# Optimization experiments

Measured on AMD Instinct MI355X. Metric: run time of the kernel, lower is better.

## Reference

```python
import jax, jax.numpy as jnp
import numpy as np

NEG_SLOPE = 0.01  # nn.LeakyReLU default


def setup_inputs() -> dict:
    key = jax.random.key(0)
    k1, k2, k3 = jax.random.split(key, 3)
    N, F_IN, F_OUT = 8192, 128, 64
    h = jax.random.normal(k1, (N, F_IN), dtype=jnp.float32)
    W = jax.random.normal(k2, (F_IN, F_OUT), dtype=jnp.float32) * (1.414 / np.sqrt(F_IN))
    a = jax.random.normal(k3, (2 * F_OUT, 1), dtype=jnp.float32) * (1.414 / np.sqrt(2 * F_OUT))
    return {"h": h, "W": W, "a": a}


def reference(h, W, a):
    # Wh: [N, F_out]
    Wh = h @ W
    F_out = W.shape[1]
    a1 = a[:F_out, 0]   # applies to the "source" (row) node i
    a2 = a[F_out:, 0]   # applies to the "target" (col) node j
    # e[i, j] = leakyrelu(a1 . Wh_i + a2 . Wh_j)  -- algebraic decomposition of
    # the concat-based score; avoids the O(N^2 * 2F) concat tensor.
    f1 = Wh @ a1  # [N]
    f2 = Wh @ a2  # [N]
    e = jax.nn.leaky_relu(f1[:, None] + f2[None, :], negative_slope=NEG_SLOPE)  # [N, N]
    attention = jax.nn.softmax(e, axis=1)
    # dropout is identity in eval mode (training=False)
    h_prime = attention @ Wh  # [N, F_out]
    return jax.nn.elu(h_prime)  # concat=True branch
```

## Files before the change

kernel.cpp:

```cpp
#include <hip/hip_runtime.h>
#include <hip/hip_bf16.h>
#include <stdint.h>

typedef float f32x4 __attribute__((ext_vector_type(4)));
typedef short s16x8 __attribute__((ext_vector_type(8)));
typedef unsigned int u32x4 __attribute__((ext_vector_type(4)));

#define L2E 1.44269504088896f

__device__ __forceinline__ unsigned short f2bf_rne(float f) {
    unsigned int u = __float_as_uint(f);
    u += 0x7fffu + ((u >> 16) & 1u);
    return (unsigned short)(u >> 16);
}

__global__ __launch_bounds__(256) void k1_wh(
    const float* __restrict__ hf,
    const float* __restrict__ Wf,
    const float* __restrict__ af,
    unsigned short* __restrict__ whT,
    float* __restrict__ f1L,
    float* __restrict__ f2L)
{
    __shared__ __align__(16) unsigned short tb[64][72];
    const int tid  = threadIdx.x;
    const int lane = tid & 63;
    const int w    = tid >> 6;
    const int col  = lane & 15;
    const int quad = lane >> 4;
    const int i0   = blockIdx.x * 64;

    f32x4 D[4];
    #pragma unroll
    for (int f = 0; f < 4; ++f) D[f] = (f32x4){0.f, 0.f, 0.f, 0.f};

    const int rowA = i0 + w * 16 + col;
    #pragma unroll
    for (int cs = 0; cs < 4; ++cs) {
        f32x4 h0 = *(const f32x4*)&hf[(size_t)rowA * 128 + cs * 32 + quad * 8];
        f32x4 h1 = *(const f32x4*)&hf[(size_t)rowA * 128 + cs * 32 + quad * 8 + 4];
        s16x8 A;
        #pragma unroll
        for (int jj = 0; jj < 4; ++jj) {
            A[jj]     = (short)f2bf_rne(h0[jj]);
            A[4 + jj] = (short)f2bf_rne(h1[jj]);
        }
        #pragma unroll
        for (int f = 0; f < 4; ++f) {
            s16x8 B;
            #pragma unroll
            for (int jj = 0; jj < 8; ++jj)
                B[jj] = (short)f2bf_rne(Wf[(cs * 32 + quad * 8 + jj) * 64 + f * 16 + col]);
            D[f] = __builtin_amdgcn_mfma_f32_16x16x32_bf16(A, B, D[f], 0, 0, 0);
        }
    }

    float a1v[4], a2v[4];
    #pragma unroll
    for (int f = 0; f < 4; ++f) {
        a1v[f] = af[f * 16 + col];
        a2v[f] = af[64 + f * 16 + col];
    }

    #pragma unroll
    for (int r = 0; r < 4; ++r) {
        float s1 = D[0][r]*a1v[0] + D[1][r]*a1v[1] + D[2][r]*a1v[2] + D[3][r]*a1v[3];
        float s2 = D[0][r]*a2v[0] + D[1][r]*a2v[1] + D[2][r]*a2v[2] + D[3][r]*a2v[3];
        #pragma unroll
        for (int d = 1; d < 16; d <<= 1) {
            s1 += __shfl_xor(s1, d, 64);
            s2 += __shfl_xor(s2, d, 64);
        }
        if (col == 0) {
            int i = i0 + w * 16 + quad * 4 + r;
            f1L[i] = s1 * L2E;
            f2L[i] = s2 * L2E;
        }
        #pragma unroll
        for (int f = 0; f < 4; ++f)
            tb[f * 16 + col][w * 16 + quad * 4 + r] = f2bf_rne(D[f][r]);
    }
    __syncthreads();
    for (int idx = tid; idx < 512; idx += 256) {
        int n = idx >> 3, c8 = (idx & 7) << 3;
        *(u32x4*)&whT[(size_t)n * 8192 + i0 + c8] = *(const u32x4*)&tb[n][c8];
    }
}

__global__ __launch_bounds__(256) void k2_attn(
    const unsigned short* __restrict__ whT,
    const float* __restrict__ f1L,
    const float* __restrict__ f2L,
    float* __restrict__ Apart,
    float* __restrict__ rsumP)
{
    __shared__ __align__(16) unsigned short Bt[64][264];
    __shared__ __align__(16) float f2s[256];
    const int tid  = threadIdx.x;
    const int lane = tid & 63;
    const int w    = tid >> 6;
    const int col  = lane & 15;
    const int quad = lane >> 4;
    const int i0   = blockIdx.x * 64;
    const int jb   = blockIdx.y * 1024;

    const float f1 = f1L[i0 + w * 16 + col];

    f32x4 D0 = (f32x4){0.f,0.f,0.f,0.f}, D1 = D0, D2 = D0, D3 = D0, Ds = D0;
    s16x8 ones;
    #pragma unroll
    for (int jj = 0; jj < 8; ++jj) ones[jj] = (short)0x3f80;

    for (int s = 0; s < 4; ++s) {
        __syncthreads();
        if (tid < 64)
            *(f32x4*)&f2s[tid * 4] = *(const f32x4*)&f2L[jb + (s << 8) + tid * 4];
        for (int idx = tid; idx < 2048; idx += 256) {
            int n = idx >> 5, c = (idx & 31) << 3;
            *(u32x4*)&Bt[n][c] =
                *(const u32x4*)&whT[(size_t)n * 8192 + jb + (s << 8) + c];
        }
        __syncthreads();
        #pragma unroll
        for (int j0 = 0; j0 < 256; j0 += 32) {
            const int jq = j0 + quad * 8;
            f32x4 fa = *(const f32x4*)&f2s[jq];
            f32x4 fb = *(const f32x4*)&f2s[jq + 4];
            unsigned int pb[8];
            #pragma unroll
            for (int e = 0; e < 4; ++e) {
                float u = f1 + fa[e];
                u = fmaxf(u, 0.01f * u);
                u = fminf(fmaxf(u, -126.f), 80.f);
                pb[e] = __float_as_uint(__builtin_amdgcn_exp2f(u));
                float v = f1 + fb[e];
                v = fmaxf(v, 0.01f * v);
                v = fminf(fmaxf(v, -126.f), 80.f);
                pb[4 + e] = __float_as_uint(__builtin_amdgcn_exp2f(v));
            }
            union { u32x4 u4; s16x8 s8; } Au;
            Au.u4[0] = __builtin_amdgcn_perm(pb[1], pb[0], 0x07060302u);
            Au.u4[1] = __builtin_amdgcn_perm(pb[3], pb[2], 0x07060302u);
            Au.u4[2] = __builtin_amdgcn_perm(pb[5], pb[4], 0x07060302u);
            Au.u4[3] = __builtin_amdgcn_perm(pb[7], pb[6], 0x07060302u);
            s16x8 B0 = *(const s16x8*)&Bt[col][jq];
            s16x8 B1 = *(const s16x8*)&Bt[16 + col][jq];
            s16x8 B2 = *(const s16x8*)&Bt[32 + col][jq];
            s16x8 B3 = *(const s16x8*)&Bt[48 + col][jq];
            D0 = __builtin_amdgcn_mfma_f32_16x16x32_bf16(Au.s8, B0, D0, 0, 0, 0);
            D1 = __builtin_amdgcn_mfma_f32_16x16x32_bf16(Au.s8, B1, D1, 0, 0, 0);
            D2 = __builtin_amdgcn_mfma_f32_16x16x32_bf16(Au.s8, B2, D2, 0, 0, 0);
            D3 = __builtin_amdgcn_mfma_f32_16x16x32_bf16(Au.s8, B3, D3, 0, 0, 0);
            Ds = __builtin_amdgcn_mfma_f32_16x16x32_bf16(Au.s8, ones, Ds, 0, 0, 0);
        }
    }

    float* Ap = Apart + (size_t)blockIdx.y * 524288;
    #pragma unroll
    for (int r = 0; r < 4; ++r) {
        int i = i0 + w * 16 + quad * 4 + r;
        Ap[(size_t)i * 64 +      col] = D0[r];
        Ap[(size_t)i * 64 + 16 + col] = D1[r];
        Ap[(size_t)i * 64 + 32 + col] = D2[r];
        Ap[(size_t)i * 64 + 48 + col] = D3[r];
        if (col == 0) rsumP[blockIdx.y * 8192 + i] = Ds[r];
    }
}

__global__ __launch_bounds__(256) void k3_combine(
    const float* __restrict__ Apart,
    const float* __restrict__ rsumP,
    float* __restrict__ out)
{
    int gid = blockIdx.x * 256 + threadIdx.x;
    int i  = gid >> 4;
    int c4 = (gid & 15) << 2;
    f32x4 num = (f32x4){0.f, 0.f, 0.f, 0.f};
    float den = 0.f;
    #pragma unroll
    for (int s = 0; s < 8; ++s) {
        num += *(const f32x4*)&Apart[(size_t)s * 524288 + (size_t)i * 64 + c4];
        den += rsumP[s * 8192 + i];
    }
    float rden = 1.f / den;
    f32x4 o;
    #pragma unroll
    for (int e = 0; e < 4; ++e) {
        float v = num[e] * rden;
        o[e] = v > 0.f ? v : (__builtin_amdgcn_exp2f(v * L2E) - 1.f);
    }
    *(f32x4*)&out[(size_t)i * 64 + c4] = o;
}

extern "C" void kernel_launch(void* const* d_in, const int* in_sizes, int n_in,
                              void* d_out, int out_size, void* d_ws, size_t ws_size,
                              hipStream_t stream) {
    const float* h = (const float*)d_in[0];
    const float* W = (const float*)d_in[1];
    const float* a = (const float*)d_in[2];
    float* out = (float*)d_out;

    char* ws = (char*)d_ws;
    unsigned short* whT = (unsigned short*)ws;
    float* f1L   = (float*)(ws + 1048576);
    float* f2L   = (float*)(ws + 1081344);
    float* Apart = (float*)(ws + 1114112);
    float* rsumP = (float*)(ws + 17891328);

    k1_wh<<<128, 256, 0, stream>>>(h, W, a, whT, f1L, f2L);
    k2_attn<<<dim3(128, 8), 256, 0, stream>>>(whT, f1L, f2L, Apart, rsumP);
    k3_combine<<<512, 256, 0, stream>>>(Apart, rsumP, out);
}
```

Baseline: 94.58 us.

## Store Wh in MFMA fragment order and stream B operands directly from global

k1 now writes the bf16 Wh in a pre-swizzled per-lane MFMA B-fragment layout, so k2 can load each B operand with one 16-byte global load per lane. That removes k2's shared-memory staging, its barriers and its LDS reads. k1 also stages a transposed bf16 copy of W in shared memory instead of doing scattered scalar global loads. The exp2 clamp is dropped, which could overflow to inf for large scores, and k2 now relies on L2/cache hits rather than LDS reuse across the four waves.

```diff
diff --git a/kernel.cpp b/kernel.cpp
--- a/kernel.cpp
+++ b/kernel.cpp
@@ -18,10 +18,11 @@
     const float* __restrict__ hf,
     const float* __restrict__ Wf,
     const float* __restrict__ af,
-    unsigned short* __restrict__ whT,
+    unsigned short* __restrict__ whB,
     float* __restrict__ f1L,
     float* __restrict__ f2L)
 {
+    __shared__ __align__(16) unsigned short Wt[64][136];
     __shared__ __align__(16) unsigned short tb[64][72];
     const int tid  = threadIdx.x;
     const int lane = tid & 63;
@@ -30,6 +31,18 @@
     const int quad = lane >> 4;
     const int i0   = blockIdx.x * 64;
 
+    #pragma unroll
+    for (int it = 0; it < 8; ++it) {
+        int fidx = tid + it * 256;
+        int k  = fidx >> 4;
+        int n4 = (fidx & 15) << 2;
+        f32x4 wv = *(const f32x4*)&Wf[k * 64 + n4];
+        #pragma unroll
+        for (int e = 0; e < 4; ++e)
+            Wt[n4 + e][k] = f2bf_rne(wv[e]);
+    }
+    __syncthreads();
+
     f32x4 D[4];
     #pragma unroll
     for (int f = 0; f < 4; ++f) D[f] = (f32x4){0.f, 0.f, 0.f, 0.f};
@@ -47,10 +60,7 @@
         }
         #pragma unroll
         for (int f = 0; f < 4; ++f) {
-            s16x8 B;
-            #pragma unroll
-            for (int jj = 0; jj < 8; ++jj)
-                B[jj] = (short)f2bf_rne(Wf[(cs * 32 + quad * 8 + jj) * 64 + f * 16 + col]);
+            s16x8 B = *(const s16x8*)&Wt[f * 16 + col][cs * 32 + quad * 8];
             D[f] = __builtin_amdgcn_mfma_f32_16x16x32_bf16(A, B, D[f], 0, 0, 0);
         }
     }
@@ -81,21 +91,25 @@
             tb[f * 16 + col][w * 16 + quad * 4 + r] = f2bf_rne(D[f][r]);
     }
     __syncthreads();
+
     for (int idx = tid; idx < 512; idx += 256) {
-        int n = idx >> 3, c8 = (idx & 7) << 3;
-        *(u32x4*)&whT[(size_t)n * 8192 + i0 + c8] = *(const u32x4*)&tb[n][c8];
+        int lane_o = idx & 63;
+        int bq     = (idx >> 6) & 3;
+        int jg_l   = idx >> 8;
+        int col_o  = lane_o & 15, quad_o = lane_o >> 4;
+        u32x4 v = *(const u32x4*)&tb[bq * 16 + col_o][jg_l * 32 + quad_o * 8];
+        size_t off = (((size_t)((i0 >> 5) + jg_l) * 4 + bq) * 64 + lane_o) * 8;
+        *(u32x4*)&whB[off] = v;
     }
 }
 
 __global__ __launch_bounds__(256) void k2_attn(
-    const unsigned short* __restrict__ whT,
+    const unsigned short* __restrict__ whB,
     const float* __restrict__ f1L,
     const float* __restrict__ f2L,
     float* __restrict__ Apart,
     float* __restrict__ rsumP)
 {
-    __shared__ __align__(16) unsigned short Bt[64][264];
-    __shared__ __align__(16) float f2s[256];
     const int tid  = threadIdx.x;
     const int lane = tid & 63;
     const int w    = tid >> 6;
@@ -111,48 +125,38 @@
     #pragma unroll
     for (int jj = 0; jj < 8; ++jj) ones[jj] = (short)0x3f80;
 
-    for (int s = 0; s < 4; ++s) {
-        __syncthreads();
-        if (tid < 64)
-            *(f32x4*)&f2s[tid * 4] = *(const f32x4*)&f2L[jb + (s << 8) + tid * 4];
-        for (int idx = tid; idx < 2048; idx += 256) {
-            int n = idx >> 5, c = (idx & 31) << 3;
-            *(u32x4*)&Bt[n][c] =
-                *(const u32x4*)&whT[(size_t)n * 8192 + jb + (s << 8) + c];
-        }
-        __syncthreads();
-        #pragma unroll
-        for (int j0 = 0; j0 < 256; j0 += 32) {
-            const int jq = j0 + quad * 8;
-            f32x4 fa = *(const f32x4*)&f2s[jq];
-            f32x4 fb = *(const f32x4*)&f2s[jq + 4];
-            unsigned int pb[8];
-            #pragma unroll
-            for (int e = 0; e < 4; ++e) {
-                float u = f1 + fa[e];
-                u = fmaxf(u, 0.01f * u);
-                u = fminf(fmaxf(u, -126.f), 80.f);
-                pb[e] = __float_as_uint(__builtin_amdgcn_exp2f(u));
-                float v = f1 + fb[e];
-                v = fmaxf(v, 0.01f * v);
-                v = fminf(fmaxf(v, -126.f), 80.f);
-                pb[4 + e] = __float_as_uint(__builtin_amdgcn_exp2f(v));
-            }
-            union { u32x4 u4; s16x8 s8; } Au;
-            Au.u4[0] = __builtin_amdgcn_perm(pb[1], pb[0], 0x07060302u);
-            Au.u4[1] = __builtin_amdgcn_perm(pb[3], pb[2], 0x07060302u);
-            Au.u4[2] = __builtin_amdgcn_perm(pb[5], pb[4], 0x07060302u);
-            Au.u4[3] = __builtin_amdgcn_perm(pb[7], pb[6], 0x07060302u);
-            s16x8 B0 = *(const s16x8*)&Bt[col][jq];
-            s16x8 B1 = *(const s16x8*)&Bt[16 + col][jq];
-            s16x8 B2 = *(const s16x8*)&Bt[32 + col][jq];
-            s16x8 B3 = *(const s16x8*)&Bt[48 + col][jq];
-            D0 = __builtin_amdgcn_mfma_f32_16x16x32_bf16(Au.s8, B0, D0, 0, 0, 0);
-            D1 = __builtin_amdgcn_mfma_f32_16x16x32_bf16(Au.s8, B1, D1, 0, 0, 0);
-            D2 = __builtin_amdgcn_mfma_f32_16x16x32_bf16(Au.s8, B2, D2, 0, 0, 0);
-            D3 = __builtin_amdgcn_mfma_f32_16x16x32_bf16(Au.s8, B3, D3, 0, 0, 0);
-            Ds = __builtin_amdgcn_mfma_f32_16x16x32_bf16(Au.s8, ones, Ds, 0, 0, 0);
-        }
+    const unsigned short* bp = whB + ((size_t)(jb >> 5) * 256 + lane) * 8;
+
+    #pragma unroll 2
+    for (int jt = 0; jt < 32; ++jt) {
+        const int jq = jb + jt * 32 + quad * 8;
+        f32x4 fa = *(const f32x4*)&f2L[jq];
+        f32x4 fb = *(const f32x4*)&f2L[jq + 4];
+        const unsigned short* bb = bp + (size_t)jt * 2048;
+        s16x8 B0 = *(const s16x8*)(bb);
+        s16x8 B1 = *(const s16x8*)(bb + 512);
+        s16x8 B2 = *(const s16x8*)(bb + 1024);
+        s16x8 B3 = *(const s16x8*)(bb + 1536);
+        unsigned int pb[8];
+        #pragma unroll
+        for (int e = 0; e < 4; ++e) {
+            float u = f1 + fa[e];
+            u = fmaxf(u, 0.01f * u);
+            pb[e] = __float_as_uint(__builtin_amdgcn_exp2f(u));
+            float v = f1 + fb[e];
+            v = fmaxf(v, 0.01f * v);
+            pb[4 + e] = __float_as_uint(__builtin_amdgcn_exp2f(v));
+        }
+        union { u32x4 u4; s16x8 s8; } Au;
+        Au.u4[0] = __builtin_amdgcn_perm(pb[1], pb[0], 0x07060302u);
+        Au.u4[1] = __builtin_amdgcn_perm(pb[3], pb[2], 0x07060302u);
+        Au.u4[2] = __builtin_amdgcn_perm(pb[5], pb[4], 0x07060302u);
+        Au.u4[3] = __builtin_amdgcn_perm(pb[7], pb[6], 0x07060302u);
+        D0 = __builtin_amdgcn_mfma_f32_16x16x32_bf16(Au.s8, B0, D0, 0, 0, 0);
+        D1 = __builtin_amdgcn_mfma_f32_16x16x32_bf16(Au.s8, B1, D1, 0, 0, 0);
+        D2 = __builtin_amdgcn_mfma_f32_16x16x32_bf16(Au.s8, B2, D2, 0, 0, 0);
+        D3 = __builtin_amdgcn_mfma_f32_16x16x32_bf16(Au.s8, B3, D3, 0, 0, 0);
+        Ds = __builtin_amdgcn_mfma_f32_16x16x32_bf16(Au.s8, ones, Ds, 0, 0, 0);
     }
 
     float* Ap = Apart + (size_t)blockIdx.y * 524288;
@@ -201,13 +205,13 @@
     float* out = (float*)d_out;
 
     char* ws = (char*)d_ws;
-    unsigned short* whT = (unsigned short*)ws;
+    unsigned short* whB = (unsigned short*)ws;
     float* f1L   = (float*)(ws + 1048576);
     float* f2L   = (float*)(ws + 1081344);
     float* Apart = (float*)(ws + 1114112);
     float* rsumP = (float*)(ws + 17891328);
 
-    k1_wh<<<128, 256, 0, stream>>>(h, W, a, whT, f1L, f2L);
-    k2_attn<<<dim3(128, 8), 256, 0, stream>>>(whT, f1L, f2L, Apart, rsumP);
+    k1_wh<<<128, 256, 0, stream>>>(h, W, a, whB, f1L, f2L);
+    k2_attn<<<dim3(128, 8), 256, 0, stream>>>(whB, f1L, f2L, Apart, rsumP);
     k3_combine<<<512, 256, 0, stream>>>(Apart, rsumP, out);
 }
```

Result: slower. 98.86 us (+4.5%).
